# Kernel optimization log

Hardware: AMD Instinct MI355X
Metric: run time of the kernel (lower is better)

Reference implementation:

```python
import jax, jax.numpy as jnp
import numpy as np

EMBED_DIM = 1024
NUM_HEADS = 16
HEAD_DIM = EMBED_DIM // NUM_HEADS
GLOBAL_HEADS = 1
LOCAL_K = 128
SCALE = HEAD_DIM ** -0.5


def setup_inputs() -> dict:
    key = jax.random.key(0)
    ks = jax.random.split(key, 9)
    B, n = 4, 2048
    s = 1.0 / np.sqrt(EMBED_DIM)  # torch Linear default uniform(-1/sqrt(in), 1/sqrt(in))
    def lin(k):
        kw, kb = jax.random.split(k)
        W = jax.random.uniform(kw, (EMBED_DIM, EMBED_DIM), jnp.float32, -s, s)
        b = jax.random.uniform(kb, (EMBED_DIM,), jnp.float32, -s, s)
        return W, b
    wq, bq = lin(ks[0])
    wk, bk = lin(ks[1])
    wv, bv = lin(ks[2])
    wo, bo = lin(ks[3])
    x = jax.random.normal(ks[4], (B, n, EMBED_DIM), jnp.float32)
    return {"x": x, "wq": wq, "bq": bq, "wk": wk, "bk": bk,
            "wv": wv, "bv": bv, "wo": wo, "bo": bo}


def _attend(x, wq, bq, wk, bk, wv, bv, wo, bo):
    B, n, E = x.shape
    H, D = NUM_HEADS, HEAD_DIM
    def proj(W, b):
        t = x @ W.T + b                       # [B, n, E]
        return t.reshape(B, n, H, D).transpose(0, 2, 1, 3)  # [B, H, n, D]
    q, k, v = proj(wq, bq), proj(wk, bk), proj(wv, bv)
    scores = jnp.einsum('bhqd,bhkd->bhqk', q, k) * SCALE  # [B, H, n, n]
    idx = jnp.arange(n)
    band = jnp.abs(idx[:, None] - idx[None, :]) <= LOCAL_K  # [n, n] True = allowed
    is_global = jnp.arange(H) < GLOBAL_HEADS
    mask = band[None, :, :] | is_global[:, None, None]      # [H, n, n]
    scores = jnp.where(mask[None], scores, -jnp.inf)
    attn = jax.nn.softmax(scores, axis=-1)   # dropout is identity (p=0 / eval)
    out = jnp.einsum('bhqk,bhkd->bhqd', attn, v)
    out = out.transpose(0, 2, 1, 3).reshape(B, n, E)
    return out @ wo.T + bo


def reference(x, wq, bq, wk, bk, wv, bv, wo, bo):
    return _attend(x, wq, bq, wk, bk, wv, bv, wo, bo)
```

## Files before the change

kernel.cpp:

```cpp
#include <hip/hip_runtime.h>

typedef __attribute__((ext_vector_type(4))) float f32x4;
typedef __attribute__((ext_vector_type(16))) float f32x16;
typedef __attribute__((ext_vector_type(8))) short s16x8;

#define GLDS(gsrc, ldst) \
  __builtin_amdgcn_global_load_lds((const __attribute__((address_space(1))) void*)(gsrc), \
                                   (__attribute__((address_space(3))) void*)(ldst), 16, 0, 0)

__device__ __forceinline__ ushort f2bf(float f) {
  union { float f; unsigned u; } x; x.f = f;
  unsigned r = (x.u + 0x7FFFu + ((x.u >> 16) & 1u)) >> 16;
  return (ushort)r;
}

__device__ __forceinline__ float fexp2(float x) {
  float r;
  asm("v_exp_f32 %0, %1" : "=v"(r) : "v"(x));
  return r;
}

__device__ __forceinline__ uint cvtpk(float a, float b) {
  uint r;
  asm("v_cvt_pk_bf16_f32 %0, %1, %2" : "=v"(r) : "v"(a), "v"(b));
  return r;
}

__device__ __forceinline__ s16x8 mk_frag(uint x0, uint x1, uint x2, uint x3) {
  union { uint u[4]; s16x8 v; } t;
  t.u[0] = x0; t.u[1] = x1; t.u[2] = x2; t.u[3] = x3;
  return t.v;
}

__global__ __launch_bounds__(256) void castall(
    const float* __restrict__ x, const float* __restrict__ wq, const float* __restrict__ wk,
    const float* __restrict__ wv, const float* __restrict__ wo,
    ushort* __restrict__ xb, ushort* __restrict__ wqkvb, ushort* __restrict__ wob) {
  int bid = blockIdx.x;
  const float* in; ushort* op;
  if (bid < 8192)       { in = x;  op = xb; }
  else if (bid < 9216)  { in = wq; op = wqkvb;           bid -= 8192; }
  else if (bid < 10240) { in = wk; op = wqkvb + 1048576; bid -= 9216; }
  else if (bid < 11264) { in = wv; op = wqkvb + 2097152; bid -= 10240; }
  else                  { in = wo; op = wob;             bid -= 11264; }
  int i = (bid * 256 + threadIdx.x) * 4;
  float4 v = *(const float4*)(in + i);
  ushort4 r;
  r.x = f2bf(v.x); r.y = f2bf(v.y); r.z = f2bf(v.z); r.w = f2bf(v.w);
  *(ushort4*)(op + i) = r;
}

template<int OUTBF16>
__global__ __launch_bounds__(512, 2) void gemm256(
    const ushort* __restrict__ A, const ushort* __restrict__ Bt,
    const float* __restrict__ bias0, const float* __restrict__ bias1,
    const float* __restrict__ bias2,
    void* __restrict__ Cout, int M, int N, int K, int nxn)
{
  __shared__ __align__(16) ushort lds[73728];
  const int tid = threadIdx.x;
  const int w = tid >> 6, lane = tid & 63;
  const int lrow = lane & 15, lg = lane >> 4;
  const int wm = w >> 2, wn = w & 3;
  const int cpx = gridDim.x >> 3;
  const int wgid = ((int)blockIdx.x & 7) * cpx + ((int)blockIdx.x >> 3);
  const int mblk = (wgid / nxn) * 128;
  const int nblk = (wgid % nxn) * 256;
  const int NT = K >> 6;

  const int srow = tid >> 3;
  const int scol = 8 * ((tid & 7) ^ (srow & 7));
  const ushort* Abase = A + (size_t)(mblk + srow) * K + scol;
  const ushort* Bbase = Bt + (size_t)(nblk + srow) * K + scol;
  const size_t rstep = (size_t)64 * K;
  const int dA = w * 512;
  const int dB = 8192 + w * 512;

#define STAGE_A(p, bf) { \
    GLDS((p),         &lds[(bf) + dA]); \
    GLDS((p) + rstep, &lds[(bf) + dA + 4096]); }
#define STAGE_B(p, bf) { \
    GLDS((p),             &lds[(bf) + dB]); \
    GLDS((p) + rstep,     &lds[(bf) + dB + 4096]); \
    GLDS((p) + 2 * rstep, &lds[(bf) + dB + 8192]); \
    GLDS((p) + 3 * rstep, &lds[(bf) + dB + 12288]); }

  const int laneA0 = (wm * 64 + lrow) * 64 + ((lg ^ (lrow & 7)) << 3);
  const int laneA1 = (wm * 64 + lrow) * 64 + (((4 + lg) ^ (lrow & 7)) << 3);
  const int laneB0 = 8192 + (wn * 64 + lrow) * 64 + ((lg ^ (lrow & 7)) << 3);
  const int laneB1 = 8192 + (wn * 64 + lrow) * 64 + (((4 + lg) ^ (lrow & 7)) << 3);

  const f32x4 zero = {0.f, 0.f, 0.f, 0.f};
  f32x4 acc[4][4];
#pragma unroll
  for (int m = 0; m < 4; m++)
#pragma unroll
    for (int n = 0; n < 4; n++) acc[m][n] = zero;

  STAGE_A(Abase, 0); STAGE_B(Bbase, 0);
  if (NT > 1) { STAGE_A(Abase + 64, 24576); STAGE_B(Bbase + 64, 24576); }

  const ushort* aP = Abase + 128;
  const ushort* bP = Bbase + 128;
  int bb = 0, bbS = 49152;

  for (int t = 0; t < NT; ++t) {
    if (t < NT - 1) { asm volatile("s_waitcnt vmcnt(6)" ::: "memory"); }
    else            { asm volatile("s_waitcnt vmcnt(0)" ::: "memory"); }
    __builtin_amdgcn_s_barrier();
    const int pA0 = bb + laneA0, pA1 = bb + laneA1;
    const int pB0 = bb + laneB0, pB1 = bb + laneB1;
    const bool pf = (t + 2 < NT);

    if (pf) STAGE_A(aP, bbS);
    {
      s16x8 af[4], bf_[4];
#pragma unroll
      for (int m = 0; m < 4; m++) af[m] = *(const s16x8*)&lds[pA0 + m * 1024];
#pragma unroll
      for (int n = 0; n < 4; n++) bf_[n] = *(const s16x8*)&lds[pB0 + n * 1024];
      __builtin_amdgcn_s_setprio(1);
#pragma unroll
      for (int m = 0; m < 4; m++)
#pragma unroll
        for (int n = 0; n < 4; n++)
          acc[m][n] = __builtin_amdgcn_mfma_f32_16x16x32_bf16(af[m], bf_[n], acc[m][n], 0, 0, 0);
      __builtin_amdgcn_s_setprio(0);
    }
    if (pf) STAGE_B(bP, bbS);
    {
      s16x8 af[4], bf_[4];
#pragma unroll
      for (int m = 0; m < 4; m++) af[m] = *(const s16x8*)&lds[pA1 + m * 1024];
#pragma unroll
      for (int n = 0; n < 4; n++) bf_[n] = *(const s16x8*)&lds[pB1 + n * 1024];
      __builtin_amdgcn_s_setprio(1);
#pragma unroll
      for (int m = 0; m < 4; m++)
#pragma unroll
        for (int n = 0; n < 4; n++)
          acc[m][n] = __builtin_amdgcn_mfma_f32_16x16x32_bf16(af[m], bf_[n], acc[m][n], 0, 0, 0);
      __builtin_amdgcn_s_setprio(0);
    }
    if (pf) { aP += 64; bP += 64; }
    bb  = (bb  == 49152) ? 0 : bb + 24576;
    bbS = (bbS == 49152) ? 0 : bbS + 24576;
  }
#undef STAGE_A
#undef STAGE_B

  float bias_n[4];
#pragma unroll
  for (int n = 0; n < 4; n++) {
    const int col = nblk + wn * 64 + n * 16 + lrow;
    if (bias1) bias_n[n] = (col < 1024) ? bias0[col]
                          : (col < 2048 ? bias1[col - 1024] : bias2[col - 2048]);
    else bias_n[n] = bias0[col];
  }

  __syncthreads();

  if (OUTBF16) {
    ushort* Ct = lds;
#pragma unroll
    for (int m = 0; m < 4; m++)
#pragma unroll
      for (int n = 0; n < 4; n++)
#pragma unroll
        for (int i = 0; i < 4; i++)
          Ct[(wm * 64 + m * 16 + 4 * lg + i) * 256 + wn * 64 + n * 16 + lrow] =
              f2bf(acc[m][n][i] + bias_n[n]);
    __syncthreads();
    ushort* Cg = (ushort*)Cout;
#pragma unroll
    for (int r = 0; r < 8; r++) {
      const int row = r * 16 + (tid >> 5);
      const int col = (tid & 31) * 8;
      *(s16x8*)&Cg[(size_t)(mblk + row) * N + nblk + col] = *(const s16x8*)&lds[r * 4096 + tid * 8];
    }
  } else {
    float* Cf = (float*)lds;
#pragma unroll
    for (int m = 0; m < 4; m++)
#pragma unroll
      for (int n = 0; n < 4; n++)
#pragma unroll
        for (int i = 0; i < 4; i++)
          Cf[(wm * 64 + m * 16 + 4 * lg + i) * 256 + wn * 64 + n * 16 + lrow] =
              acc[m][n][i] + bias_n[n];
    __syncthreads();
    float* Cg = (float*)Cout;
#pragma unroll
    for (int r = 0; r < 16; r++) {
      const int row = r * 8 + (tid >> 6);
      const int col = (tid & 63) * 4;
      *(float4*)&Cg[(size_t)(mblk + row) * N + nblk + col] = *(const float4*)&Cf[r * 2048 + tid * 4];
    }
  }
}

__global__ __launch_bounds__(256, 2) void attn_kernel(const ushort* __restrict__ qkv,
                                                      ushort* __restrict__ outp,
                                                      float* __restrict__ oPart,
                                                      float* __restrict__ mPart,
                                                      float* __restrict__ lPart)
{
  __shared__ __align__(16) ushort Ks[2][4096];
  __shared__ __align__(16) ushort Vt[2][4096];

  const int tid = threadIdx.x;
  const int w = tid >> 6, lane = tid & 63;
  const int lq = lane & 31, hi = lane >> 5;
  const float NINF = -__builtin_inff();

  const int bid = (blockIdx.x & 7) * 184 + (blockIdx.x >> 3);
  int h, b, bx, kv_lo, kv_hi, chunk = 0;
  bool isGlobal;
  if (bid < 512) {
    isGlobal = true; h = 0;
    chunk = bid >> 6;
    int qb = bid & 63;
    b = qb >> 4; bx = qb & 15;
    kv_lo = chunk * 256; kv_hi = kv_lo + 256;
  } else {
    isGlobal = false;
    int t = bid - 512;
    h = 1 + (t >> 6);
    int qb = t & 63;
    b = qb >> 4; bx = qb & 15;
    kv_lo = bx * 128 - 128; if (kv_lo < 0) kv_lo = 0;
    kv_hi = bx * 128 + 256; if (kv_hi > 2048) kv_hi = 2048;
  }
  const int q0blk = bx * 128;
  const int qw = q0blk + 32 * w;
  const int q_abs = qw + lq;
  const ushort* Qp = qkv + (size_t)b * 2048 * 3072 + h * 64;
  const ushort* Kp = Qp + 1024;
  const ushort* Vp = Qp + 2048;

  s16x8 qf[4];
#pragma unroll
  for (int c = 0; c < 4; c++)
    qf[c] = *(const s16x8*)(Qp + (size_t)q_abs * 3072 + 16 * c + 8 * hi);

  f32x16 o0, o1;
#pragma unroll
  for (int r = 0; r < 16; r++) { o0[r] = 0.f; o1[r] = 0.f; }
  float mrun = -3e38f, lsum = 0.f;
  const float SCL = 0.18033688011112042f;

  const int kg = lane >> 3;
  const int kswz = 8 * ((lane & 7) ^ kg);
  const int krow0 = 16 * w + kg;
  const int vsp = tid >> 3;
  const int vsg = tid & 7;

  const ushort* vr0 = Vp + (size_t)(kv_lo + 2 * vsp) * 3072 + 8 * vsg;
  s16x8 v0 = *(const s16x8*)vr0;
  s16x8 v1 = *(const s16x8*)(vr0 + 3072);
  GLDS(Kp + (size_t)(kv_lo + krow0) * 3072 + kswz,     &Ks[0][(2 * w) * 512]);
  GLDS(Kp + (size_t)(kv_lo + krow0 + 8) * 3072 + kswz, &Ks[0][(2 * w + 1) * 512]);

  int buf = 0;
  for (int kv = kv_lo; kv < kv_hi; kv += 64) {
    const bool hasNext = (kv + 64 < kv_hi);
    const bool active = isGlobal || ((kv + 63 >= qw - 128) && (kv <= qw + 159));
    const bool needMask = !isGlobal && active && ((kv < qw - 97) || (kv > qw + 65));

    s16x8 vn0, vn1;
    if (hasNext) {
      const ushort* vr = Vp + (size_t)(kv + 64 + 2 * vsp) * 3072 + 8 * vsg;
      vn0 = *(const s16x8*)vr;
      vn1 = *(const s16x8*)(vr + 3072);
    }

#pragma unroll
    for (int j = 0; j < 8; j++) {
      const int d = 8 * vsg + j;
      const int sl = ((vsp >> 2) ^ j ^ vsg) & 7;
      *(uint*)&Vt[buf][d * 64 + sl * 8 + ((2 * vsp) & 7)] =
          (uint)(ushort)v0[j] | ((uint)(ushort)v1[j] << 16);
    }
    if (hasNext) asm volatile("s_waitcnt vmcnt(2)" ::: "memory");
    else         asm volatile("s_waitcnt vmcnt(0)" ::: "memory");
    asm volatile("s_waitcnt lgkmcnt(0)" ::: "memory");
    __builtin_amdgcn_s_barrier();
    if (hasNext) {
      GLDS(Kp + (size_t)(kv + 64 + krow0) * 3072 + kswz,     &Ks[buf ^ 1][(2 * w) * 512]);
      GLDS(Kp + (size_t)(kv + 64 + krow0 + 8) * 3072 + kswz, &Ks[buf ^ 1][(2 * w + 1) * 512]);
    }

    if (active) {
      f32x16 s0, s1;
#pragma unroll
      for (int r = 0; r < 16; r++) { s0[r] = 0.f; s1[r] = 0.f; }
#pragma unroll
      for (int c = 0; c < 4; c++) {
        const int gx = ((2 * c + hi) ^ (lq & 7)) << 3;
        s16x8 kf0 = *(const s16x8*)&Ks[buf][lq * 64 + gx];
        s16x8 kf1 = *(const s16x8*)&Ks[buf][(32 + lq) * 64 + gx];
        s0 = __builtin_amdgcn_mfma_f32_32x32x16_bf16(kf0, qf[c], s0, 0, 0, 0);
        s1 = __builtin_amdgcn_mfma_f32_32x32x16_bf16(kf1, qf[c], s1, 0, 0, 0);
      }

      float rm = NINF;
      if (needMask) {
#pragma unroll
        for (int r = 0; r < 16; r++) {
          const int kvr = kv + (r & 3) + 8 * (r >> 2) + 4 * hi;
          const int dq0 = q_abs - kvr;
          s0[r] = (dq0 <= 128 && dq0 >= -128) ? s0[r] : NINF;
          const int dq1 = dq0 - 32;
          s1[r] = (dq1 <= 128 && dq1 >= -128) ? s1[r] : NINF;
          rm = fmaxf(rm, fmaxf(s0[r], s1[r]));
        }
      } else {
#pragma unroll
        for (int r = 0; r < 16; r++) rm = fmaxf(rm, fmaxf(s0[r], s1[r]));
      }
      rm = fmaxf(rm, __shfl_xor(rm, 32)) * SCL;

      if (!__all(rm <= mrun + 8.f)) {
        float mnew = fmaxf(mrun, rm);
        float alpha = fexp2(mrun - mnew);
        mrun = mnew;
        lsum *= alpha;
#pragma unroll
        for (int r = 0; r < 16; r++) {
          float av = __shfl(alpha, (r & 3) + 8 * (r >> 2) + 4 * hi);
          o0[r] *= av; o1[r] *= av;
        }
      }

      float rs = 0.f;
#pragma unroll
      for (int r = 0; r < 16; r++) {
        s0[r] = fexp2(__builtin_fmaf(s0[r], SCL, -mrun)); rs += s0[r];
        s1[r] = fexp2(__builtin_fmaf(s1[r], SCL, -mrun)); rs += s1[r];
      }
      rs += __shfl_xor(rs, 32);
      lsum += rs;

#pragma unroll
      for (int cc = 0; cc < 4; cc++) {
        uint x0, x1, x2, x3;
        if (cc == 0) { x0 = cvtpk(s0[0], s0[1]);  x1 = cvtpk(s0[2], s0[3]);
                       x2 = cvtpk(s0[4], s0[5]);  x3 = cvtpk(s0[6], s0[7]); }
        else if (cc == 1) { x0 = cvtpk(s0[8], s0[9]);   x1 = cvtpk(s0[10], s0[11]);
                            x2 = cvtpk(s0[12], s0[13]); x3 = cvtpk(s0[14], s0[15]); }
        else if (cc == 2) { x0 = cvtpk(s1[0], s1[1]);  x1 = cvtpk(s1[2], s1[3]);
                            x2 = cvtpk(s1[4], s1[5]);  x3 = cvtpk(s1[6], s1[7]); }
        else { x0 = cvtpk(s1[8], s1[9]);   x1 = cvtpk(s1[10], s1[11]);
               x2 = cvtpk(s1[12], s1[13]); x3 = cvtpk(s1[14], s1[15]); }
        uint t0 = hi ? x0 : x2;
        uint t1 = hi ? x1 : x3;
        uint r0 = __shfl_xor(t0, 32);
        uint r1 = __shfl_xor(t1, 32);
        uint w0 = hi ? r0 : x0;
        uint w1 = hi ? r1 : x1;
        uint w2 = hi ? x2 : r0;
        uint w3 = hi ? x3 : r1;
        s16x8 pa = mk_frag(w0, w1, w2, w3);
#pragma unroll
        for (int db = 0; db < 2; db++) {
          const int d = 32 * db + lq;
          s16x8 vf = *(const s16x8*)&Vt[buf][d * 64 +
              ((((2 * cc + hi) ^ (d & 7) ^ (d >> 3)) & 7) << 3)];
          if (db == 0) o0 = __builtin_amdgcn_mfma_f32_32x32x16_bf16(pa, vf, o0, 0, 0, 0);
          else         o1 = __builtin_amdgcn_mfma_f32_32x32x16_bf16(pa, vf, o1, 0, 0, 0);
        }
      }
    }

    v0 = vn0; v1 = vn1;
    buf ^= 1;
  }

  if (isGlobal) {
    const size_t rq = (size_t)(chunk * 4 + b) * 2048 + qw;
    if (hi == 0) {
      mPart[rq + lq] = mrun;
      lPart[rq + lq] = lsum;
    }
#pragma unroll
    for (int r = 0; r < 16; r++) {
      const int qr = (r & 3) + 8 * (r >> 2) + 4 * hi;
      oPart[(rq + qr) * 64 + lq]      = o0[r];
      oPart[(rq + qr) * 64 + 32 + lq] = o1[r];
    }
  } else {
    float linv = 1.f / lsum;
#pragma unroll
    for (int r = 0; r < 16; r++) {
      const int qr = (r & 3) + 8 * (r >> 2) + 4 * hi;
      float iv = __shfl(linv, qr);
      size_t orow = (size_t)(b * 2048 + qw + qr) * 1024 + h * 64;
      outp[orow + lq]      = f2bf(o0[r] * iv);
      outp[orow + 32 + lq] = f2bf(o1[r] * iv);
    }
  }
}

__global__ __launch_bounds__(256) void combine_kernel(const float* __restrict__ oPart,
                                                      const float* __restrict__ mPart,
                                                      const float* __restrict__ lPart,
                                                      ushort* __restrict__ attno) {
  const int tid = threadIdx.x;
  const int row = blockIdx.x * 64 + (tid >> 2);
  const int d0 = (tid & 3) * 16;
  float m[8], l[8], M = -3e38f;
#pragma unroll
  for (int p = 0; p < 8; p++) {
    m[p] = mPart[p * 8192 + row];
    l[p] = lPart[p * 8192 + row];
    M = fmaxf(M, m[p]);
  }
  float L = 0.f, wgt[8];
#pragma unroll
  for (int p = 0; p < 8; p++) { wgt[p] = fexp2(m[p] - M); L += wgt[p] * l[p]; }
  float inv = 1.f / L;
  float acc[16];
#pragma unroll
  for (int j = 0; j < 16; j++) acc[j] = 0.f;
#pragma unroll
  for (int p = 0; p < 8; p++) {
    const float* op = oPart + ((size_t)p * 8192 + row) * 64 + d0;
    float wv = wgt[p];
#pragma unroll
    for (int j = 0; j < 16; j += 4) {
      float4 v = *(const float4*)(op + j);
      acc[j]     += wv * v.x; acc[j + 1] += wv * v.y;
      acc[j + 2] += wv * v.z; acc[j + 3] += wv * v.w;
    }
  }
  ushort* dst = attno + (size_t)row * 1024 + d0;
#pragma unroll
  for (int j = 0; j < 16; j++) dst[j] = f2bf(acc[j] * inv);
}

extern "C" void kernel_launch(void* const* d_in, const int* in_sizes, int n_in,
                              void* d_out, int out_size, void* d_ws, size_t ws_size,
                              hipStream_t stream) {
  const float* x  = (const float*)d_in[0];
  const float* wq = (const float*)d_in[1];
  const float* bq = (const float*)d_in[2];
  const float* wk = (const float*)d_in[3];
  const float* bk = (const float*)d_in[4];
  const float* wv = (const float*)d_in[5];
  const float* bv = (const float*)d_in[6];
  const float* wo = (const float*)d_in[7];
  const float* bo = (const float*)d_in[8];

  char* ws = (char*)d_ws;
  ushort* xb    = (ushort*)(ws);
  ushort* wqkvb = (ushort*)(ws + 16777216);
  ushort* wob   = (ushort*)(ws + 23068672);
  ushort* qkvb  = (ushort*)(ws + 25165824);
  ushort* attno = (ushort*)(ws + 75497472);
  float* oPart = (float*)(ws);
  float* mPart = (float*)(ws + 16777216);
  float* lPart = (float*)(ws + 16777216 + 262144);

  castall<<<12288, 256, 0, stream>>>(x, wq, wk, wv, wo, xb, wqkvb, wob);

  gemm256<1><<<768, 512, 0, stream>>>(xb, wqkvb, bq, bk, bv,
                                      (void*)qkvb, 8192, 3072, 1024, 12);

  attn_kernel<<<1472, 256, 0, stream>>>(qkvb, attno, oPart, mPart, lPart);
  combine_kernel<<<128, 256, 0, stream>>>(oPart, mPart, lPart, attno);

  gemm256<0><<<256, 512, 0, stream>>>(attno, wob, bo, nullptr, nullptr,
                                      (void*)d_out, 8192, 1024, 1024, 4);
}
```

Baseline: 153.2 us.

## Replace 128x256 pipelined GEMM with simpler 128x128 single-buffered GEMM

Replaces the 512-thread, 128x256-tile, triple-buffered GEMM with a 256-thread, 128x128-tile kernel that loads a K=32 slab into small LDS and synchronises twice per step. It launches twice as many workgroups and uses far less LDS, so more blocks can be resident and the grid spreads more evenly across CUs. The cost is losing the async prefetch/compute overlap and getting less data reuse per tile. The attention kernel also gets s_setprio around its MFMA blocks.

```diff
diff --git a/kernel.cpp b/kernel.cpp
--- a/kernel.cpp
+++ b/kernel.cpp
@@ -51,44 +51,32 @@
 }
 
 template<int OUTBF16>
-__global__ __launch_bounds__(512, 2) void gemm256(
+__global__ __launch_bounds__(256) void gemm128(
     const ushort* __restrict__ A, const ushort* __restrict__ Bt,
     const float* __restrict__ bias0, const float* __restrict__ bias1,
     const float* __restrict__ bias2,
     void* __restrict__ Cout, int M, int N, int K, int nxn)
 {
-  __shared__ __align__(16) ushort lds[73728];
+  __shared__ __align__(16) ushort lds[16384];
   const int tid = threadIdx.x;
   const int w = tid >> 6, lane = tid & 63;
   const int lrow = lane & 15, lg = lane >> 4;
-  const int wm = w >> 2, wn = w & 3;
+  const int wm = w >> 1, wn = w & 1;
   const int cpx = gridDim.x >> 3;
   const int wgid = ((int)blockIdx.x & 7) * cpx + ((int)blockIdx.x >> 3);
   const int mblk = (wgid / nxn) * 128;
-  const int nblk = (wgid % nxn) * 256;
-  const int NT = K >> 6;
-
-  const int srow = tid >> 3;
-  const int scol = 8 * ((tid & 7) ^ (srow & 7));
-  const ushort* Abase = A + (size_t)(mblk + srow) * K + scol;
-  const ushort* Bbase = Bt + (size_t)(nblk + srow) * K + scol;
-  const size_t rstep = (size_t)64 * K;
-  const int dA = w * 512;
-  const int dB = 8192 + w * 512;
-
-#define STAGE_A(p, bf) { \
-    GLDS((p),         &lds[(bf) + dA]); \
-    GLDS((p) + rstep, &lds[(bf) + dA + 4096]); }
-#define STAGE_B(p, bf) { \
-    GLDS((p),             &lds[(bf) + dB]); \
-    GLDS((p) + rstep,     &lds[(bf) + dB + 4096]); \
-    GLDS((p) + 2 * rstep, &lds[(bf) + dB + 8192]); \
-    GLDS((p) + 3 * rstep, &lds[(bf) + dB + 12288]); }
-
-  const int laneA0 = (wm * 64 + lrow) * 64 + ((lg ^ (lrow & 7)) << 3);
-  const int laneA1 = (wm * 64 + lrow) * 64 + (((4 + lg) ^ (lrow & 7)) << 3);
-  const int laneB0 = 8192 + (wn * 64 + lrow) * 64 + ((lg ^ (lrow & 7)) << 3);
-  const int laneB1 = 8192 + (wn * 64 + lrow) * 64 + (((4 + lg) ^ (lrow & 7)) << 3);
+  const int nblk = (wgid % nxn) * 128;
+
+  const int srow = tid >> 2;
+  const int scol = 8 * ((tid & 3) ^ (srow & 3));
+  const ushort* Ab = A + (size_t)(mblk + srow) * K + scol;
+  const ushort* Bb = Bt + (size_t)(nblk + srow) * K + scol;
+  const size_t r64 = (size_t)64 * K;
+  const int wb = w * 512;
+
+  const int xk = (lg ^ (lrow & 3)) << 3;
+  const int laneA = (wm * 64 + lrow) * 32 + xk;
+  const int laneB = 4096 + (wn * 64 + lrow) * 32 + xk;
 
   const f32x4 zero = {0.f, 0.f, 0.f, 0.f};
   f32x4 acc[4][4];
@@ -97,57 +85,26 @@
 #pragma unroll
     for (int n = 0; n < 4; n++) acc[m][n] = zero;
 
-  STAGE_A(Abase, 0); STAGE_B(Bbase, 0);
-  if (NT > 1) { STAGE_A(Abase + 64, 24576); STAGE_B(Bbase + 64, 24576); }
-
-  const ushort* aP = Abase + 128;
-  const ushort* bP = Bbase + 128;
-  int bb = 0, bbS = 49152;
-
-  for (int t = 0; t < NT; ++t) {
-    if (t < NT - 1) { asm volatile("s_waitcnt vmcnt(6)" ::: "memory"); }
-    else            { asm volatile("s_waitcnt vmcnt(0)" ::: "memory"); }
-    __builtin_amdgcn_s_barrier();
-    const int pA0 = bb + laneA0, pA1 = bb + laneA1;
-    const int pB0 = bb + laneB0, pB1 = bb + laneB1;
-    const bool pf = (t + 2 < NT);
-
-    if (pf) STAGE_A(aP, bbS);
-    {
-      s16x8 af[4], bf_[4];
-#pragma unroll
-      for (int m = 0; m < 4; m++) af[m] = *(const s16x8*)&lds[pA0 + m * 1024];
-#pragma unroll
-      for (int n = 0; n < 4; n++) bf_[n] = *(const s16x8*)&lds[pB0 + n * 1024];
-      __builtin_amdgcn_s_setprio(1);
-#pragma unroll
-      for (int m = 0; m < 4; m++)
-#pragma unroll
-        for (int n = 0; n < 4; n++)
-          acc[m][n] = __builtin_amdgcn_mfma_f32_16x16x32_bf16(af[m], bf_[n], acc[m][n], 0, 0, 0);
-      __builtin_amdgcn_s_setprio(0);
-    }
-    if (pf) STAGE_B(bP, bbS);
-    {
-      s16x8 af[4], bf_[4];
-#pragma unroll
-      for (int m = 0; m < 4; m++) af[m] = *(const s16x8*)&lds[pA1 + m * 1024];
-#pragma unroll
-      for (int n = 0; n < 4; n++) bf_[n] = *(const s16x8*)&lds[pB1 + n * 1024];
-      __builtin_amdgcn_s_setprio(1);
-#pragma unroll
-      for (int m = 0; m < 4; m++)
-#pragma unroll
-        for (int n = 0; n < 4; n++)
-          acc[m][n] = __builtin_amdgcn_mfma_f32_16x16x32_bf16(af[m], bf_[n], acc[m][n], 0, 0, 0);
-      __builtin_amdgcn_s_setprio(0);
-    }
-    if (pf) { aP += 64; bP += 64; }
-    bb  = (bb  == 49152) ? 0 : bb + 24576;
-    bbS = (bbS == 49152) ? 0 : bbS + 24576;
-  }
-#undef STAGE_A
-#undef STAGE_B
+  for (int kt = 0; kt < K; kt += 32) {
+    GLDS(Ab + kt,       &lds[wb]);
+    GLDS(Ab + kt + r64, &lds[2048 + wb]);
+    GLDS(Bb + kt,       &lds[4096 + wb]);
+    GLDS(Bb + kt + r64, &lds[6144 + wb]);
+    __syncthreads();
+    s16x8 af[4], bf_[4];
+#pragma unroll
+    for (int m = 0; m < 4; m++) af[m] = *(const s16x8*)&lds[laneA + m * 512];
+#pragma unroll
+    for (int n = 0; n < 4; n++) bf_[n] = *(const s16x8*)&lds[laneB + n * 512];
+    __builtin_amdgcn_s_setprio(1);
+#pragma unroll
+    for (int m = 0; m < 4; m++)
+#pragma unroll
+      for (int n = 0; n < 4; n++)
+        acc[m][n] = __builtin_amdgcn_mfma_f32_16x16x32_bf16(af[m], bf_[n], acc[m][n], 0, 0, 0);
+    __builtin_amdgcn_s_setprio(0);
+    __syncthreads();
+  }
 
   float bias_n[4];
 #pragma unroll
@@ -158,43 +115,51 @@
     else bias_n[n] = bias0[col];
   }
 
-  __syncthreads();
-
-  if (OUTBF16) {
+  if constexpr (OUTBF16) {
     ushort* Ct = lds;
 #pragma unroll
     for (int m = 0; m < 4; m++)
 #pragma unroll
-      for (int n = 0; n < 4; n++)
+      for (int n = 0; n < 4; n++) {
+        f32x4 v = acc[m][n];
 #pragma unroll
         for (int i = 0; i < 4; i++)
-          Ct[(wm * 64 + m * 16 + 4 * lg + i) * 256 + wn * 64 + n * 16 + lrow] =
-              f2bf(acc[m][n][i] + bias_n[n]);
+          Ct[(wm * 64 + m * 16 + 4 * lg + i) * 128 + wn * 64 + n * 16 + lrow] =
+              f2bf(v[i] + bias_n[n]);
+      }
     __syncthreads();
     ushort* Cg = (ushort*)Cout;
 #pragma unroll
-    for (int r = 0; r < 8; r++) {
-      const int row = r * 16 + (tid >> 5);
-      const int col = (tid & 31) * 8;
-      *(s16x8*)&Cg[(size_t)(mblk + row) * N + nblk + col] = *(const s16x8*)&lds[r * 4096 + tid * 8];
+    for (int p = 0; p < 8; p++) {
+      const unsigned g = p * 256 + tid;
+      const unsigned row = g >> 4, c8 = g & 15;
+      *(s16x8*)&Cg[(size_t)(mblk + row) * N + nblk + c8 * 8] = *(const s16x8*)&lds[g * 8];
     }
   } else {
     float* Cf = (float*)lds;
-#pragma unroll
-    for (int m = 0; m < 4; m++)
-#pragma unroll
-      for (int n = 0; n < 4; n++)
-#pragma unroll
-        for (int i = 0; i < 4; i++)
-          Cf[(wm * 64 + m * 16 + 4 * lg + i) * 256 + wn * 64 + n * 16 + lrow] =
-              acc[m][n][i] + bias_n[n];
-    __syncthreads();
     float* Cg = (float*)Cout;
 #pragma unroll
-    for (int r = 0; r < 16; r++) {
-      const int row = r * 8 + (tid >> 6);
-      const int col = (tid & 63) * 4;
-      *(float4*)&Cg[(size_t)(mblk + row) * N + nblk + col] = *(const float4*)&Cf[r * 2048 + tid * 4];
+    for (int ch = 0; ch < 2; ch++) {
+      __syncthreads();
+      if (wm == ch) {
+#pragma unroll
+        for (int m = 0; m < 4; m++)
+#pragma unroll
+          for (int n = 0; n < 4; n++) {
+            f32x4 v = acc[m][n];
+#pragma unroll
+            for (int i = 0; i < 4; i++)
+              Cf[(m * 16 + 4 * lg + i) * 128 + wn * 64 + n * 16 + lrow] = v[i] + bias_n[n];
+          }
+      }
+      __syncthreads();
+#pragma unroll
+      for (int p = 0; p < 8; p++) {
+        const unsigned fg = p * 256 + tid;
+        const unsigned row = fg >> 5, c4 = fg & 31;
+        *(float4*)&Cg[(size_t)(mblk + ch * 64 + row) * N + nblk + c4 * 4] =
+            *(const float4*)&Cf[fg * 4];
+      }
     }
   }
 }
@@ -294,6 +259,7 @@
       f32x16 s0, s1;
 #pragma unroll
       for (int r = 0; r < 16; r++) { s0[r] = 0.f; s1[r] = 0.f; }
+      __builtin_amdgcn_s_setprio(1);
 #pragma unroll
       for (int c = 0; c < 4; c++) {
         const int gx = ((2 * c + hi) ^ (lq & 7)) << 3;
@@ -302,6 +268,7 @@
         s0 = __builtin_amdgcn_mfma_f32_32x32x16_bf16(kf0, qf[c], s0, 0, 0, 0);
         s1 = __builtin_amdgcn_mfma_f32_32x32x16_bf16(kf1, qf[c], s1, 0, 0, 0);
       }
+      __builtin_amdgcn_s_setprio(0);
 
       float rm = NINF;
       if (needMask) {
@@ -361,6 +328,7 @@
         uint w2 = hi ? x2 : r0;
         uint w3 = hi ? x3 : r1;
         s16x8 pa = mk_frag(w0, w1, w2, w3);
+        __builtin_amdgcn_s_setprio(1);
 #pragma unroll
         for (int db = 0; db < 2; db++) {
           const int d = 32 * db + lq;
@@ -369,6 +337,7 @@
           if (db == 0) o0 = __builtin_amdgcn_mfma_f32_32x32x16_bf16(pa, vf, o0, 0, 0, 0);
           else         o1 = __builtin_amdgcn_mfma_f32_32x32x16_bf16(pa, vf, o1, 0, 0, 0);
         }
+        __builtin_amdgcn_s_setprio(0);
       }
     }
 
@@ -463,12 +432,12 @@
 
   castall<<<12288, 256, 0, stream>>>(x, wq, wk, wv, wo, xb, wqkvb, wob);
 
-  gemm256<1><<<768, 512, 0, stream>>>(xb, wqkvb, bq, bk, bv,
-                                      (void*)qkvb, 8192, 3072, 1024, 12);
+  gemm128<1><<<1536, 256, 0, stream>>>(xb, wqkvb, bq, bk, bv,
+                                       (void*)qkvb, 8192, 3072, 1024, 24);
 
   attn_kernel<<<1472, 256, 0, stream>>>(qkvb, attno, oPart, mPart, lPart);
   combine_kernel<<<128, 256, 0, stream>>>(oPart, mPart, lPart, attno);
 
-  gemm256<0><<<256, 512, 0, stream>>>(attno, wob, bo, nullptr, nullptr,
-                                      (void*)d_out, 8192, 1024, 1024, 4);
-}
+  gemm128<0><<<512, 256, 0, stream>>>(attno, wob, bo, nullptr, nullptr,
+                                      (void*)d_out, 8192, 1024, 1024, 8);
+}
```

New measurement: 162.9 us. +6.4%, slower.
